# Kernel optimization log

Hardware: AMD Instinct MI355X
Metric: run time of the kernel (lower is better)

Reference implementation:

```python
import jax, jax.numpy as jnp
import numpy as np

EMBED = 1024
HEADS = 16
HEAD_DIM = EMBED // HEADS


def setup_inputs() -> dict:
    key = jax.random.key(0)
    k1, k2, k3 = jax.random.split(key, 3)
    B, T = 4, 2048
    query = jax.random.normal(k1, (B, T, EMBED), dtype=jnp.float32)
    # xavier-ish scaled weights
    in_proj_w = jax.random.normal(k2, (3 * EMBED, EMBED), dtype=jnp.float32) * (1.0 / np.sqrt(EMBED))
    in_proj_b = jnp.zeros((3 * EMBED,), dtype=jnp.float32)
    out_proj_w = jax.random.normal(k3, (EMBED, EMBED), dtype=jnp.float32) * (1.0 / np.sqrt(EMBED))
    out_proj_b = jnp.zeros((EMBED,), dtype=jnp.float32)
    return {"query": query, "in_proj_w": in_proj_w, "in_proj_b": in_proj_b,
            "out_proj_w": out_proj_w, "out_proj_b": out_proj_b}


def reference(query, in_proj_w, in_proj_b, out_proj_w, out_proj_b):
    # Self-attention (qkv_same path), batch_first=True, dropout=0 (eval).
    B, T, E = query.shape
    H, D = HEADS, HEAD_DIM
    scaling = D ** -0.5
    # fused QKV projection: [B,T,3E]
    qkv = jnp.einsum('bte,fe->btf', query, in_proj_w) + in_proj_b
    q, k, v = jnp.split(qkv, 3, axis=-1)
    q = q * scaling
    # reshape to [B,H,T,D]
    q = q.reshape(B, T, H, D).transpose(0, 2, 1, 3)
    k = k.reshape(B, T, H, D).transpose(0, 2, 1, 3)
    v = v.reshape(B, T, H, D).transpose(0, 2, 1, 3)
    scores = jnp.einsum('bhqd,bhkd->bhqk', q, k)
    attn = jax.nn.softmax(scores, axis=-1)
    ctx = jnp.einsum('bhqk,bhkd->bhqd', attn, v)  # [B,H,T,D]
    ctx = ctx.transpose(0, 2, 1, 3).reshape(B, T, E)
    out = jnp.einsum('bte,fe->btf', ctx, out_proj_w) + out_proj_b
    return out
```

## Files before the change

kernel.cpp:

```cpp
#include <hip/hip_runtime.h>
#include <math.h>

using bf16x8 = __attribute__((ext_vector_type(8))) short;
using f32x4  = __attribute__((ext_vector_type(4))) float;
using u16x8  = __attribute__((ext_vector_type(8))) unsigned short;
using u16x4  = __attribute__((ext_vector_type(4))) unsigned short;

constexpr int Bb = 4, Tt = 2048, Ee = 1024, Hh = 16;
constexpr int Mm = Bb * Tt;
constexpr int E3 = 3 * Ee;

__device__ __forceinline__ unsigned short f2bf(float f) {
  union { float f; unsigned int u; } c; c.f = f;
  unsigned int u = c.u;
  u += 0x7fffu + ((u >> 16) & 1u);
  return (unsigned short)(u >> 16);
}

__device__ __forceinline__ f32x4 mfma16(bf16x8 a, bf16x8 b, f32x4 c) {
  return __builtin_amdgcn_mfma_f32_16x16x32_bf16(a, b, c, 0, 0, 0);
}

__device__ __forceinline__ void gload_lds16(const unsigned short* g, unsigned short* l) {
  __builtin_amdgcn_global_load_lds(
      (const __attribute__((address_space(1))) unsigned int*)g,
      (__attribute__((address_space(3))) unsigned int*)l, 16, 0, 0);
}

__global__ void cvt_f32_bf16(const float* __restrict__ in, unsigned short* __restrict__ out, int n8) {
  const int i = blockIdx.x * 256 + threadIdx.x;
  if (i >= n8) return;
  const float4* p = (const float4*)in + (size_t)i * 2;
  const float4 a = p[0], b = p[1];
  u16x8 r = { f2bf(a.x), f2bf(a.y), f2bf(a.z), f2bf(a.w),
              f2bf(b.x), f2bf(b.y), f2bf(b.z), f2bf(b.w) };
  *(u16x8*)(out + (size_t)i * 8) = r;
}

template <bool OUT_BF16, bool QSCALE>
__global__ __launch_bounds__(256, 2)
void gemm_bt(const unsigned short* __restrict__ A, const unsigned short* __restrict__ Bw,
             const float* __restrict__ bias, void* __restrict__ Cout, int N, int K) {
  __shared__ alignas(16) unsigned short As[128 * 32];
  __shared__ alignas(16) unsigned short Bs[128 * 32];
  const int tid = threadIdx.x;
  const int wave = tid >> 6, lane = tid & 63;
  const int l15 = lane & 15, quad = lane >> 4;
  const int wr = wave >> 1, wc = wave & 1;
  const int row0 = blockIdx.y * 128, col0 = blockIdx.x * 128;
  const int srow = lane >> 2, sslot = lane & 3;

  f32x4 acc[4][4];
#pragma unroll
  for (int i = 0; i < 4; ++i)
#pragma unroll
    for (int j = 0; j < 4; ++j) acc[i][j] = f32x4{0.f, 0.f, 0.f, 0.f};

  for (int k0 = 0; k0 < K; k0 += 32) {
#pragma unroll
    for (int t = 0; t < 2; ++t) {
      const int rA = wave * 32 + t * 16 + srow;
      const int g = sslot ^ ((rA >> 1) & 3);
      gload_lds16(A  + (size_t)(row0 + rA) * K + k0 + g * 8, &As[(wave * 32 + t * 16) * 32]);
      gload_lds16(Bw + (size_t)(col0 + rA) * K + k0 + g * 8, &Bs[(wave * 32 + t * 16) * 32]);
    }
    __syncthreads();

    bf16x8 af[4], bfr[4];
#pragma unroll
    for (int mi = 0; mi < 4; ++mi) {
      const int m = wr * 64 + mi * 16 + l15;
      af[mi] = *(const bf16x8*)&As[m * 32 + (quad ^ ((m >> 1) & 3)) * 8];
    }
#pragma unroll
    for (int ni = 0; ni < 4; ++ni) {
      const int n = wc * 64 + ni * 16 + l15;
      bfr[ni] = *(const bf16x8*)&Bs[n * 32 + (quad ^ ((n >> 1) & 3)) * 8];
    }
#pragma unroll
    for (int mi = 0; mi < 4; ++mi)
#pragma unroll
      for (int ni = 0; ni < 4; ++ni) acc[mi][ni] = mfma16(af[mi], bfr[ni], acc[mi][ni]);
    __syncthreads();
  }

#pragma unroll
  for (int mi = 0; mi < 4; ++mi)
#pragma unroll
    for (int ni = 0; ni < 4; ++ni) {
      const int col = col0 + wc * 64 + ni * 16 + l15;
      const float bv = bias[col];
#pragma unroll
      for (int r = 0; r < 4; ++r) {
        const int row = row0 + wr * 64 + mi * 16 + quad * 4 + r;
        float v = acc[mi][ni][r] + bv;
        if (QSCALE && col < 1024) v *= 0.125f;
        if (OUT_BF16)
          ((unsigned short*)Cout)[(size_t)row * N + col] = f2bf(v);
        else
          ((float*)Cout)[(size_t)row * N + col] = v;
      }
    }
}

__global__ __launch_bounds__(256, 2)
void attn_mfma(const unsigned short* __restrict__ qkv, unsigned short* __restrict__ ctx) {
  __shared__ alignas(16) unsigned short Vt[64][72];
  __shared__ alignas(16) unsigned short Ps[128][72];
  const int tid = threadIdx.x;
  const int wave = tid >> 6, lane = tid & 63;
  const int l15 = lane & 15, quad = lane >> 4;
  const int b = blockIdx.x >> 4, h = blockIdx.x & 15;
  const int q0 = blockIdx.y * 128;

  bf16x8 qa[2][2];
#pragma unroll
  for (int mi = 0; mi < 2; ++mi)
#pragma unroll
    for (int kf = 0; kf < 2; ++kf)
      qa[mi][kf] = *(const bf16x8*)(qkv +
          (size_t)(b * Tt + q0 + wave * 32 + mi * 16 + l15) * E3 + h * 64 + kf * 32 + quad * 8);

  f32x4 o[2][4];
  float lp[2][4];
#pragma unroll
  for (int mi = 0; mi < 2; ++mi) {
#pragma unroll
    for (int di = 0; di < 4; ++di) o[mi][di] = f32x4{0.f, 0.f, 0.f, 0.f};
#pragma unroll
    for (int r = 0; r < 4; ++r) lp[mi][r] = 0.f;
  }

  const int jb = (tid & 15) * 4, db = (tid >> 4) * 4;

  for (int j0 = 0; j0 < Tt; j0 += 64) {
    {
      u16x4 vr[4];
#pragma unroll
      for (int r = 0; r < 4; ++r)
        vr[r] = *(const u16x4*)(qkv + (size_t)(b * Tt + j0 + jb + r) * E3 + 2 * Ee + h * 64 + db);
#pragma unroll
      for (int c = 0; c < 4; ++c) {
        u16x4 w = { vr[0][c], vr[1][c], vr[2][c], vr[3][c] };
        *(u16x4*)&Vt[db + c][jb] = w;
      }
    }
    __syncthreads();

    f32x4 s[2][4];
#pragma unroll
    for (int ni = 0; ni < 4; ++ni) {
      const size_t krow = (size_t)(b * Tt + j0 + ni * 16 + l15) * E3 + Ee + h * 64 + quad * 8;
      const bf16x8 kb0 = *(const bf16x8*)(qkv + krow);
      const bf16x8 kb1 = *(const bf16x8*)(qkv + krow + 32);
#pragma unroll
      for (int mi = 0; mi < 2; ++mi) {
        s[mi][ni] = mfma16(qa[mi][0], kb0, f32x4{0.f, 0.f, 0.f, 0.f});
        s[mi][ni] = mfma16(qa[mi][1], kb1, s[mi][ni]);
      }
    }

#pragma unroll
    for (int mi = 0; mi < 2; ++mi)
#pragma unroll
      for (int ni = 0; ni < 4; ++ni)
#pragma unroll
        for (int r = 0; r < 4; ++r) {
          const float p = __expf(s[mi][ni][r]);
          lp[mi][r] += p;
          Ps[wave * 32 + mi * 16 + quad * 4 + r][ni * 16 + l15] = f2bf(p);
        }
    __asm__ volatile("s_waitcnt lgkmcnt(0)" ::: "memory");

    bf16x8 pa[2][2], vb[4][2];
#pragma unroll
    for (int mi = 0; mi < 2; ++mi)
#pragma unroll
      for (int kf = 0; kf < 2; ++kf)
        pa[mi][kf] = *(const bf16x8*)&Ps[wave * 32 + mi * 16 + l15][kf * 32 + quad * 8];
#pragma unroll
    for (int di = 0; di < 4; ++di)
#pragma unroll
      for (int kf = 0; kf < 2; ++kf)
        vb[di][kf] = *(const bf16x8*)&Vt[di * 16 + l15][kf * 32 + quad * 8];
#pragma unroll
    for (int mi = 0; mi < 2; ++mi)
#pragma unroll
      for (int di = 0; di < 4; ++di) {
        o[mi][di] = mfma16(pa[mi][0], vb[di][0], o[mi][di]);
        o[mi][di] = mfma16(pa[mi][1], vb[di][1], o[mi][di]);
      }
    __syncthreads();
  }

  float inv[2][4];
#pragma unroll
  for (int mi = 0; mi < 2; ++mi)
#pragma unroll
    for (int r = 0; r < 4; ++r) {
      float v = lp[mi][r];
      v += __shfl_xor(v, 1, 64);
      v += __shfl_xor(v, 2, 64);
      v += __shfl_xor(v, 4, 64);
      v += __shfl_xor(v, 8, 64);
      inv[mi][r] = 1.0f / v;
    }
#pragma unroll
  for (int mi = 0; mi < 2; ++mi)
#pragma unroll
    for (int di = 0; di < 4; ++di)
#pragma unroll
      for (int r = 0; r < 4; ++r)
        ctx[(size_t)(b * Tt + q0 + wave * 32 + mi * 16 + quad * 4 + r) * Ee + h * 64 + di * 16 + l15] =
            f2bf(o[mi][di][r] * inv[mi][r]);
}

extern "C" void kernel_launch(void* const* d_in, const int* in_sizes, int n_in,
                              void* d_out, int out_size, void* d_ws, size_t ws_size,
                              hipStream_t stream) {
  const float* query = (const float*)d_in[0];
  const float* in_w  = (const float*)d_in[1];
  const float* in_b  = (const float*)d_in[2];
  const float* out_w = (const float*)d_in[3];
  const float* out_b = (const float*)d_in[4];
  float* out = (float*)d_out;

  char* w = (char*)d_ws;
  unsigned short* qkvb = (unsigned short*)(w);
  unsigned short* ctxb = (unsigned short*)(w + 50331648);
  unsigned short* qb   = (unsigned short*)(w + 67108864);
  unsigned short* wib  = (unsigned short*)(w + 83886080);
  unsigned short* wob  = (unsigned short*)(w + 90177536);

  cvt_f32_bf16<<<4096, 256, 0, stream>>>(query, qb, (Mm * Ee) / 8);
  cvt_f32_bf16<<<1536, 256, 0, stream>>>(in_w, wib, (E3 * Ee) / 8);
  cvt_f32_bf16<<<512, 256, 0, stream>>>(out_w, wob, (Ee * Ee) / 8);

  gemm_bt<true, true><<<dim3(E3 / 128, Mm / 128), 256, 0, stream>>>(qb, wib, in_b, qkvb, E3, Ee);
  attn_mfma<<<dim3(Bb * Hh, Tt / 128), 256, 0, stream>>>(qkvb, ctxb);
  gemm_bt<false, false><<<dim3(Ee / 128, Mm / 128), 256, 0, stream>>>(ctxb, wob, out_b, out, Ee, Ee);
}
```

Before: 369.9 us.

## Pre-transpose V and restructure attention to per-wave 64-query tiles without block syncs

Adds a separate kernel that transposes V into a [bh, D, T] buffer, so the attention kernel reads V fragments directly from global memory instead of transposing them in shared memory each iteration. The attention kernel now gives each wave its own 64 queries and a private P scratch area, which removes the __syncthreads calls. It folds log2(e) into the Q scale so exp2 can be used, packs P to bf16 by truncation, and computes the row sums with an MFMA against a ones vector instead of scalar adds and shuffles. The cost is an extra kernel launch plus a V transpose round-trip through memory, higher register pressure, and slightly different rounding of P.

```diff
diff --git a/kernel.cpp b/kernel.cpp
--- a/kernel.cpp
+++ b/kernel.cpp
@@ -90,11 +90,11 @@
     for (int ni = 0; ni < 4; ++ni) {
       const int col = col0 + wc * 64 + ni * 16 + l15;
       const float bv = bias[col];
+      const float scale = (QSCALE && col < 1024) ? 0.18033688f : 1.0f;
 #pragma unroll
       for (int r = 0; r < 4; ++r) {
         const int row = row0 + wr * 64 + mi * 16 + quad * 4 + r;
-        float v = acc[mi][ni][r] + bv;
-        if (QSCALE && col < 1024) v *= 0.125f;
+        float v = (acc[mi][ni][r] + bv) * scale;
         if (OUT_BF16)
           ((unsigned short*)Cout)[(size_t)row * N + col] = f2bf(v);
         else
@@ -104,115 +104,129 @@
 }
 
 __global__ __launch_bounds__(256, 2)
-void attn_mfma(const unsigned short* __restrict__ qkv, unsigned short* __restrict__ ctx) {
-  __shared__ alignas(16) unsigned short Vt[64][72];
-  __shared__ alignas(16) unsigned short Ps[128][72];
+void transpose_v(const unsigned short* __restrict__ qkv, unsigned short* __restrict__ vt) {
+  __shared__ unsigned short L[128][66];
+  const int tid = threadIdx.x;
+  const int bh = blockIdx.x, b = bh >> 4, h = bh & 15;
+  const int t0 = blockIdx.y * 128;
+#pragma unroll
+  for (int p = 0; p < 8; ++p) {
+    const int tl = p * 16 + (tid >> 4);
+    const int d = (tid & 15) * 4;
+    *(u16x4*)&L[tl][d] = *(const u16x4*)(qkv + (size_t)(b * Tt + t0 + tl) * E3 + 2 * Ee + h * 64 + d);
+  }
+  __syncthreads();
+#pragma unroll
+  for (int p = 0; p < 8; ++p) {
+    const int dw = (tid >> 5) * 8 + p;
+    const int tw = (tid & 31) * 4;
+    u16x4 w = { L[tw][dw], L[tw + 1][dw], L[tw + 2][dw], L[tw + 3][dw] };
+    *(u16x4*)(vt + ((size_t)bh * 64 + dw) * Tt + t0 + tw) = w;
+  }
+}
+
+__global__ __launch_bounds__(256, 2)
+void attn_mfma2(const unsigned short* __restrict__ qkv,
+                const unsigned short* __restrict__ vt,
+                unsigned short* __restrict__ ctx) {
+  __shared__ alignas(16) unsigned short Ps[4 * 4096];
   const int tid = threadIdx.x;
   const int wave = tid >> 6, lane = tid & 63;
   const int l15 = lane & 15, quad = lane >> 4;
-  const int b = blockIdx.x >> 4, h = blockIdx.x & 15;
-  const int q0 = blockIdx.y * 128;
-
-  bf16x8 qa[2][2];
-#pragma unroll
-  for (int mi = 0; mi < 2; ++mi)
+  const int bh = blockIdx.x, b = bh >> 4, h = bh & 15;
+  const int q0 = blockIdx.y * 256 + wave * 64;
+  unsigned short* const ps = &Ps[wave * 4096];
+  const int swz = l15 & 14;
+
+  bf16x8 qa[4][2];
+#pragma unroll
+  for (int qi = 0; qi < 4; ++qi)
 #pragma unroll
     for (int kf = 0; kf < 2; ++kf)
-      qa[mi][kf] = *(const bf16x8*)(qkv +
-          (size_t)(b * Tt + q0 + wave * 32 + mi * 16 + l15) * E3 + h * 64 + kf * 32 + quad * 8);
-
-  f32x4 o[2][4];
-  float lp[2][4];
-#pragma unroll
-  for (int mi = 0; mi < 2; ++mi) {
-#pragma unroll
-    for (int di = 0; di < 4; ++di) o[mi][di] = f32x4{0.f, 0.f, 0.f, 0.f};
-#pragma unroll
-    for (int r = 0; r < 4; ++r) lp[mi][r] = 0.f;
-  }
-
-  const int jb = (tid & 15) * 4, db = (tid >> 4) * 4;
-
-  for (int j0 = 0; j0 < Tt; j0 += 64) {
-    {
-      u16x4 vr[4];
+      qa[qi][kf] = *(const bf16x8*)(qkv +
+          (size_t)(b * Tt + q0 + qi * 16 + l15) * E3 + h * 64 + kf * 32 + quad * 8);
+
+  f32x4 o[4][4], ol[4];
+#pragma unroll
+  for (int qi = 0; qi < 4; ++qi) {
+    ol[qi] = f32x4{0.f, 0.f, 0.f, 0.f};
+#pragma unroll
+    for (int di = 0; di < 4; ++di) o[qi][di] = f32x4{0.f, 0.f, 0.f, 0.f};
+  }
+  bf16x8 ones;
+#pragma unroll
+  for (int i = 0; i < 8; ++i) ones[i] = (short)0x3F80;
+
+  const unsigned short* kp = qkv + (size_t)(b * Tt + l15) * E3 + Ee + h * 64 + quad * 8;
+  const unsigned short* vp = vt + ((size_t)bh * 64 + l15) * Tt + quad * 8;
+
+  for (int it = 0; it < Tt / 64; ++it) {
+    bf16x8 vb[4][2], kb[4][2];
+#pragma unroll
+    for (int di = 0; di < 4; ++di)
+#pragma unroll
+      for (int kf = 0; kf < 2; ++kf)
+        vb[di][kf] = *(const bf16x8*)(vp + di * 16 * Tt + kf * 32);
+#pragma unroll
+    for (int ki = 0; ki < 4; ++ki)
+#pragma unroll
+      for (int kf = 0; kf < 2; ++kf)
+        kb[ki][kf] = *(const bf16x8*)(kp + (size_t)ki * 16 * E3 + kf * 32);
+
+#pragma unroll
+    for (int ki = 0; ki < 4; ++ki) {
+      f32x4 s[4];
+#pragma unroll
+      for (int qi = 0; qi < 4; ++qi) {
+        s[qi] = mfma16(kb[ki][0], qa[qi][0], f32x4{0.f, 0.f, 0.f, 0.f});
+        s[qi] = mfma16(kb[ki][1], qa[qi][1], s[qi]);
+      }
+#pragma unroll
+      for (int qi = 0; qi < 4; ++qi) {
+        const float e0 = __builtin_amdgcn_exp2f(s[qi][0]);
+        const float e1 = __builtin_amdgcn_exp2f(s[qi][1]);
+        const float e2 = __builtin_amdgcn_exp2f(s[qi][2]);
+        const float e3 = __builtin_amdgcn_exp2f(s[qi][3]);
+        uint2 w;
+        w.x = __builtin_amdgcn_perm(__float_as_uint(e1), __float_as_uint(e0), 0x07060302u);
+        w.y = __builtin_amdgcn_perm(__float_as_uint(e3), __float_as_uint(e2), 0x07060302u);
+        *(uint2*)(ps + (qi * 16 + l15) * 64 + (((ki * 4 + quad) ^ swz) << 2)) = w;
+      }
+    }
+    __asm__ volatile("s_waitcnt lgkmcnt(0)" ::: "memory");
+
+    bf16x8 pa[4][2];
+#pragma unroll
+    for (int qi = 0; qi < 4; ++qi)
+#pragma unroll
+      for (int kf = 0; kf < 2; ++kf)
+        pa[qi][kf] = *(const bf16x8*)(ps + (qi * 16 + l15) * 64 + (((kf * 8 + quad * 2) ^ swz) << 2));
+#pragma unroll
+    for (int qi = 0; qi < 4; ++qi) {
+      ol[qi] = mfma16(pa[qi][0], ones, ol[qi]);
+      ol[qi] = mfma16(pa[qi][1], ones, ol[qi]);
+#pragma unroll
+      for (int di = 0; di < 4; ++di) {
+        o[qi][di] = mfma16(pa[qi][0], vb[di][0], o[qi][di]);
+        o[qi][di] = mfma16(pa[qi][1], vb[di][1], o[qi][di]);
+      }
+    }
+    kp += 64 * E3;
+    vp += 64;
+  }
+
+#pragma unroll
+  for (int qi = 0; qi < 4; ++qi) {
+    f32x4 inv;
+#pragma unroll
+    for (int r = 0; r < 4; ++r) inv[r] = 1.0f / ol[qi][r];
+#pragma unroll
+    for (int di = 0; di < 4; ++di)
 #pragma unroll
       for (int r = 0; r < 4; ++r)
-        vr[r] = *(const u16x4*)(qkv + (size_t)(b * Tt + j0 + jb + r) * E3 + 2 * Ee + h * 64 + db);
-#pragma unroll
-      for (int c = 0; c < 4; ++c) {
-        u16x4 w = { vr[0][c], vr[1][c], vr[2][c], vr[3][c] };
-        *(u16x4*)&Vt[db + c][jb] = w;
-      }
-    }
-    __syncthreads();
-
-    f32x4 s[2][4];
-#pragma unroll
-    for (int ni = 0; ni < 4; ++ni) {
-      const size_t krow = (size_t)(b * Tt + j0 + ni * 16 + l15) * E3 + Ee + h * 64 + quad * 8;
-      const bf16x8 kb0 = *(const bf16x8*)(qkv + krow);
-      const bf16x8 kb1 = *(const bf16x8*)(qkv + krow + 32);
-#pragma unroll
-      for (int mi = 0; mi < 2; ++mi) {
-        s[mi][ni] = mfma16(qa[mi][0], kb0, f32x4{0.f, 0.f, 0.f, 0.f});
-        s[mi][ni] = mfma16(qa[mi][1], kb1, s[mi][ni]);
-      }
-    }
-
-#pragma unroll
-    for (int mi = 0; mi < 2; ++mi)
-#pragma unroll
-      for (int ni = 0; ni < 4; ++ni)
-#pragma unroll
-        for (int r = 0; r < 4; ++r) {
-          const float p = __expf(s[mi][ni][r]);
-          lp[mi][r] += p;
-          Ps[wave * 32 + mi * 16 + quad * 4 + r][ni * 16 + l15] = f2bf(p);
-        }
-    __asm__ volatile("s_waitcnt lgkmcnt(0)" ::: "memory");
-
-    bf16x8 pa[2][2], vb[4][2];
-#pragma unroll
-    for (int mi = 0; mi < 2; ++mi)
-#pragma unroll
-      for (int kf = 0; kf < 2; ++kf)
-        pa[mi][kf] = *(const bf16x8*)&Ps[wave * 32 + mi * 16 + l15][kf * 32 + quad * 8];
-#pragma unroll
-    for (int di = 0; di < 4; ++di)
-#pragma unroll
-      for (int kf = 0; kf < 2; ++kf)
-        vb[di][kf] = *(const bf16x8*)&Vt[di * 16 + l15][kf * 32 + quad * 8];
-#pragma unroll
-    for (int mi = 0; mi < 2; ++mi)
-#pragma unroll
-      for (int di = 0; di < 4; ++di) {
-        o[mi][di] = mfma16(pa[mi][0], vb[di][0], o[mi][di]);
-        o[mi][di] = mfma16(pa[mi][1], vb[di][1], o[mi][di]);
-      }
-    __syncthreads();
-  }
-
-  float inv[2][4];
-#pragma unroll
-  for (int mi = 0; mi < 2; ++mi)
-#pragma unroll
-    for (int r = 0; r < 4; ++r) {
-      float v = lp[mi][r];
-      v += __shfl_xor(v, 1, 64);
-      v += __shfl_xor(v, 2, 64);
-      v += __shfl_xor(v, 4, 64);
-      v += __shfl_xor(v, 8, 64);
-      inv[mi][r] = 1.0f / v;
-    }
-#pragma unroll
-  for (int mi = 0; mi < 2; ++mi)
-#pragma unroll
-    for (int di = 0; di < 4; ++di)
-#pragma unroll
-      for (int r = 0; r < 4; ++r)
-        ctx[(size_t)(b * Tt + q0 + wave * 32 + mi * 16 + quad * 4 + r) * Ee + h * 64 + di * 16 + l15] =
-            f2bf(o[mi][di][r] * inv[mi][r]);
+        ctx[(size_t)(b * Tt + q0 + qi * 16 + quad * 4 + r) * Ee + h * 64 + di * 16 + l15] =
+            f2bf(o[qi][di][r] * inv[r]);
+  }
 }
 
 extern "C" void kernel_launch(void* const* d_in, const int* in_sizes, int n_in,
@@ -231,12 +245,14 @@
   unsigned short* qb   = (unsigned short*)(w + 67108864);
   unsigned short* wib  = (unsigned short*)(w + 83886080);
   unsigned short* wob  = (unsigned short*)(w + 90177536);
+  unsigned short* vtb  = (unsigned short*)(w + 92274688);
 
   cvt_f32_bf16<<<4096, 256, 0, stream>>>(query, qb, (Mm * Ee) / 8);
   cvt_f32_bf16<<<1536, 256, 0, stream>>>(in_w, wib, (E3 * Ee) / 8);
   cvt_f32_bf16<<<512, 256, 0, stream>>>(out_w, wob, (Ee * Ee) / 8);
 
   gemm_bt<true, true><<<dim3(E3 / 128, Mm / 128), 256, 0, stream>>>(qb, wib, in_b, qkvb, E3, Ee);
-  attn_mfma<<<dim3(Bb * Hh, Tt / 128), 256, 0, stream>>>(qkvb, ctxb);
+  transpose_v<<<dim3(Bb * Hh, Tt / 128), 256, 0, stream>>>(qkvb, vtb);
+  attn_mfma2<<<dim3(Bb * Hh, Tt / 256), 256, 0, stream>>>(qkvb, vtb, ctxb);
   gemm_bt<false, false><<<dim3(Ee / 128, Mm / 128), 256, 0, stream>>>(ctxb, wob, out_b, out, Ee, Ee);
 }
```

New measurement: 317.9 us. 14.1% less time.
